# Optimization experiments

Hardware: AMD Instinct MI355X
Metric: run time of the kernel (lower is better)

## Reference

```python
import jax, jax.numpy as jnp
import numpy as np

N_CH = 62
F_DIM = 16
T_DIM = 32
B_DIM = 256
N_NODES = B_DIM * N_CH  # 15872
E_DIM = 200000
SEQ = T_DIM * F_DIM  # 512


def setup_inputs() -> dict:
    key = jax.random.key(0)
    ks = iter(jax.random.split(key, 40))
    s = 0.05
    inp = {}
    inp['x'] = jax.random.normal(next(ks), (N_NODES, F_DIM, T_DIM), dtype=jnp.float32)
    inp['edge_index'] = jax.random.randint(next(ks), (T_DIM, 2, E_DIM), 0, N_NODES, dtype=jnp.int64)
    inp['edge_weight'] = jax.random.uniform(next(ks), (T_DIM, E_DIM), dtype=jnp.float32)
    inp['batch'] = jax.random.randint(next(ks), (T_DIM, N_NODES), 0, B_DIM, dtype=jnp.int64)
    # ChebConv params (K=2): lins have no bias, single bias added at end
    for p in ['c1', 'c2']:
        inp[p + '_w0'] = jax.random.normal(next(ks), (F_DIM, F_DIM), dtype=jnp.float32) * s
        inp[p + '_w1'] = jax.random.normal(next(ks), (F_DIM, F_DIM), dtype=jnp.float32) * s
        inp[p + '_b'] = jnp.zeros((F_DIM,), jnp.float32)
    # LSTM params (torch gate order i,f,g,o); fold b_ih+b_hh into one bias
    for name, i_dim, h_dim in [('l1', N_CH, 64), ('l2', 64, 128), ('l3', 128, 256)]:
        inp[name + '_wih'] = jax.random.normal(next(ks), (4 * h_dim, i_dim), dtype=jnp.float32) * s
        inp[name + '_whh'] = jax.random.normal(next(ks), (4 * h_dim, h_dim), dtype=jnp.float32) * s
        inp[name + '_b'] = jnp.zeros((4 * h_dim,), jnp.float32)
    # MLP head
    for name, i_dim, o_dim in [('fc1', SEQ * 256, 256), ('fc2', 256, 128), ('fc3', 128, 64), ('fc4', 64, 4)]:
        inp[name + '_w'] = jax.random.normal(next(ks), (i_dim, o_dim), dtype=jnp.float32) * s
        inp[name + '_b'] = jnp.zeros((o_dim,), jnp.float32)
    return inp


def _cheb(x, src, dst, w, w0, w1, b):
    # PyG ChebConv K=2, sym norm, lambda_max=2: Tx1 = -D^{-1/2} A D^{-1/2} x
    n = x.shape[0]
    deg = jax.ops.segment_sum(w, src, num_segments=n)
    dinv = jnp.where(deg > 0, jax.lax.rsqrt(deg), 0.0)
    norm = -dinv[src] * w * dinv[dst]
    tx1 = jax.ops.segment_sum(norm[:, None] * x[src], dst, num_segments=n)
    return x @ w0 + tx1 @ w1 + b


def _lstm(x, wih, whh, b):
    # x: [B, S, I] -> [B, S, H], batch_first, zero init state
    bsz, _, _ = x.shape
    h_dim = whh.shape[1]
    xg = x @ wih.T + b  # precompute input gates [B, S, 4H]
    def step(carry, xt):
        h, c = carry
        g = xt + h @ whh.T
        i, f, gg, o = jnp.split(g, 4, axis=-1)
        c = jax.nn.sigmoid(f) * c + jax.nn.sigmoid(i) * jnp.tanh(gg)
        h = jax.nn.sigmoid(o) * jnp.tanh(c)
        return (h, c), h
    h0 = jnp.zeros((bsz, h_dim), x.dtype)
    _, hs = jax.lax.scan(step, (h0, h0), jnp.swapaxes(xg, 0, 1))
    return jnp.swapaxes(hs, 0, 1)


def reference(x, edge_index, edge_weight, batch,
              c1_w0, c1_w1, c1_b, c2_w0, c2_w1, c2_b,
              l1_wih, l1_whh, l1_b, l2_wih, l2_whh, l2_b, l3_wih, l3_whh, l3_b,
              fc1_w, fc1_b, fc2_w, fc2_b, fc3_w, fc3_b, fc4_w, fc4_b):
    def per_t(xt, ei, w):
        h = _cheb(xt, ei[0], ei[1], w, c1_w0, c1_w1, c1_b)
        h = jax.nn.leaky_relu(h, 0.01)
        return _cheb(h, ei[0], ei[1], w, c2_w0, c2_w1, c2_b)
    xt_first = jnp.moveaxis(x, -1, 0)  # [T, N, F]
    h = jax.vmap(per_t)(xt_first, edge_index, edge_weight)  # [T, N, F]
    xc = jnp.moveaxis(h, 0, -1)  # [N, F, T]
    xc = xc.reshape(B_DIM, N_CH, F_DIM, T_DIM)
    xc = jnp.transpose(xc, (0, 3, 2, 1))  # [B, T, F, 62]
    xc = xc.reshape(B_DIM, T_DIM * F_DIM, N_CH)  # [B, S, 62]
    h = _lstm(xc, l1_wih, l1_whh, l1_b)
    h = _lstm(h, l2_wih, l2_whh, l2_b)
    h = _lstm(h, l3_wih, l3_whh, l3_b)
    z = h.reshape(B_DIM, -1)  # [B, S*256]
    z = jax.nn.relu(z @ fc1_w + fc1_b)
    z = jax.nn.relu(z @ fc2_w + fc2_b)
    z = jax.nn.relu(z @ fc3_w + fc3_b)
    return z @ fc4_w + fc4_b
```

## Files before the change

kernel.cpp:

```cpp
#include <hip/hip_runtime.h>
#include <cstdint>
#include <cstddef>


#define T_DIM 32
#define F_DIMC 16
#define NNODE 15872
#define EDGES 200000
#define BATCH 256
#define SEQL 512
#define TN (T_DIM * NNODE)
#define TE (T_DIM * EDGES)
#define ESEG 25000

typedef unsigned short ushortT;
typedef __bf16 bf16_t;
typedef bf16_t bf16x8 __attribute__((ext_vector_type(8)));
typedef float f32x4 __attribute__((ext_vector_type(4)));

__device__ __forceinline__ ushortT f2bf(float f) {
  union { float f; unsigned u; } v; v.f = f;
  unsigned u = v.u;
  u += 0x7fffu + ((u >> 16) & 1u);
  return (ushortT)(u >> 16);
}
__device__ __forceinline__ float fsig(float x) { return 1.0f / (1.0f + __expf(-x)); }
__device__ __forceinline__ float ftanh(float x) {
  float e = __expf(2.0f * x);
  return 1.0f - 2.0f / (e + 1.0f);
}
#define PIN(v) asm volatile("" : "+v"(v))

__device__ __forceinline__ void bar_sync() {
  asm volatile("s_waitcnt lgkmcnt(0)\n\ts_barrier" ::: "memory");
  __builtin_amdgcn_sched_barrier(0);
}

__global__ void k_wprep(const float* __restrict__ w1i, const float* __restrict__ w1h,
                        const float* __restrict__ w2i, const float* __restrict__ w2h,
                        const float* __restrict__ w3i, const float* __restrict__ w3h,
                        ushortT* __restrict__ Wcat) {
  int id = blockIdx.x * 256 + threadIdx.x;
  if (id >= 524288) return;
  float v;
  if (id < 32768) {
    int g = id >> 7, k = id & 127;
    v = (k < 62) ? w1i[g * 62 + k] : ((k >= 64) ? w1h[g * 64 + (k - 64)] : 0.0f);
  } else if (id < 131072) {
    int j = id - 32768; int g = j / 192, k = j % 192;
    v = (k < 64) ? w2i[g * 64 + k] : w2h[g * 128 + (k - 64)];
  } else {
    int j = id - 131072; int g = j / 384, k = j % 384;
    v = (k < 128) ? w3i[g * 128 + k] : w3h[g * 256 + (k - 128)];
  }
  Wcat[id] = f2bf(v);
}

__global__ void k_transpose(const float* __restrict__ x, float* __restrict__ xt) {
  __shared__ float s[528];
  int n = blockIdx.x;
  int tid = threadIdx.x;
  for (int i = tid; i < 512; i += 256) {
    s[(i >> 5) * 33 + (i & 31)] = x[(size_t)n * 512 + i];
  }
  __syncthreads();
  for (int i = tid; i < 512; i += 256) {
    int t = i >> 4, f = i & 15;
    xt[((size_t)t * NNODE + n) * 16 + f] = s[f * 33 + t];
  }
}

__global__ __launch_bounds__(1024, 1) void k_hist8(const int* __restrict__ ei,
                                                   const float* __restrict__ ew,
                                                   float* __restrict__ pdeg,
                                                   int* __restrict__ pcnt,
                                                   int* __restrict__ rank) {
  __shared__ float sdeg[NNODE];
  __shared__ int scnt[NNODE];
  int t = blockIdx.x >> 3;
  int b = blockIdx.x & 7;
  int tid = threadIdx.x;
  for (int i = tid; i < NNODE; i += 1024) { sdeg[i] = 0.0f; scnt[i] = 0; }
  __syncthreads();
  const int* srcp = ei + (size_t)(2 * t) * EDGES;
  const int* dstp = ei + (size_t)(2 * t + 1) * EDGES;
  const float* ewp = ew + (size_t)t * EDGES;
  int* rankp = rank + (size_t)t * EDGES;
  int e0 = b * ESEG, e1 = e0 + ESEG;
  for (int e = e0 + tid; e < e1; e += 1024) {
    int src = srcp[e];
    int dst = dstp[e];
    float w = ewp[e];
    atomicAdd(&sdeg[src], w);
    rankp[e] = atomicAdd(&scnt[dst], 1);
  }
  __syncthreads();
  float* pd = pdeg + (size_t)blockIdx.x * NNODE;
  int* pc = pcnt + (size_t)blockIdx.x * NNODE;
  for (int i = tid; i < NNODE; i += 1024) {
    pd[i] = sdeg[i];
    pc[i] = scnt[i];
  }
}

__global__ void k_merge(const float* __restrict__ pdeg, const int* __restrict__ pcnt,
                        float* __restrict__ deg, int* __restrict__ counts,
                        int* __restrict__ bko) {
  int gid = blockIdx.x * 256 + threadIdx.x;
  if (gid >= TN) return;
  int t = gid / NNODE, n = gid % NNODE;
  int base = t * 8;
  float d = 0.0f;
  int s = 0;
  int pref[8];
#pragma unroll
  for (int b = 0; b < 8; ++b) {
    pref[b] = s;
    d += pdeg[(size_t)(base + b) * NNODE + n];
    s += pcnt[(size_t)(base + b) * NNODE + n];
  }
#pragma unroll
  for (int b = 0; b < 8; ++b) bko[(size_t)gid * 8 + b] = pref[b];
  deg[gid] = d;
  counts[gid] = s;
}

__global__ void k_scanA(const int* __restrict__ counts, int* __restrict__ offs,
                        int* __restrict__ ctot, float* __restrict__ deg) {
  __shared__ int s[256];
  int tid = threadIdx.x;
  int gid = blockIdx.x * 256 + tid;
  float d = deg[gid];
  int v = counts[gid];
  s[tid] = v; __syncthreads();
  for (int off = 1; off < 256; off <<= 1) {
    int x = (tid >= off) ? s[tid - off] : 0;
    __syncthreads();
    s[tid] += x;
    __syncthreads();
  }
  offs[gid] = s[tid] - v;
  if (tid == 255) ctot[blockIdx.x] = s[255];
  deg[gid] = (d > 0.0f) ? rsqrtf(d) : 0.0f;
}

__global__ void k_scanB(const int* __restrict__ ctot, int* __restrict__ cbase) {
  __shared__ int s[256];
  int tid = threadIdx.x;
  int carry = 0;
  for (int c = 0; c < 8; ++c) {
    int i = c * 256 + tid;
    int v = (i < 1984) ? ctot[i] : 0;
    s[tid] = v; __syncthreads();
    for (int off = 1; off < 256; off <<= 1) {
      int x = (tid >= off) ? s[tid - off] : 0;
      __syncthreads();
      s[tid] += x;
      __syncthreads();
    }
    if (i < 1984) cbase[i] = carry + s[tid] - v;
    int tot = s[255];
    __syncthreads();
    carry += tot;
  }
}

__global__ void k_fill2(const int* __restrict__ ei, const float* __restrict__ ew,
                        const float* __restrict__ dinv, const int* __restrict__ offs,
                        const int* __restrict__ cbase, const int* __restrict__ bko,
                        const int* __restrict__ rank,
                        int* __restrict__ csrs, float* __restrict__ csrn) {
  int id = blockIdx.x * 256 + threadIdx.x;
  if (id >= TE) return;
  int t = id / EDGES, e = id % EDGES;
  int src = ei[(size_t)(2 * t) * EDGES + e];
  int dst = ei[(size_t)(2 * t + 1) * EDGES + e];
  int idx = t * NNODE + dst;
  int seg = e / ESEG;
  int pos = offs[idx] + cbase[idx >> 8] + bko[(size_t)idx * 8 + seg] + rank[id];
  csrs[pos] = src;
  csrn[pos] = -dinv[t * NNODE + src] * ew[id] * dinv[idx];
}

__device__ __forceinline__ void fma4(float4& a, float sc, const float4 b) {
  a.x += sc * b.x; a.y += sc * b.y; a.z += sc * b.z; a.w += sc * b.w;
}

__global__ void k_gc(const float* __restrict__ in, const int* __restrict__ offs,
                     const int* __restrict__ cbase,
                     const int* __restrict__ csrs, const float* __restrict__ csrn,
                     const float* __restrict__ w0, const float* __restrict__ w1,
                     const float* __restrict__ bias, float* __restrict__ outF,
                     ushortT* __restrict__ outX, int mode) {
  __shared__ float sw0[256], sw1[256], sb[16];
  int tid = threadIdx.x;
  sw0[tid] = w0[tid];
  sw1[tid] = w1[tid];
  if (tid < 16) sb[tid] = bias[tid];
  __syncthreads();
  int idx = blockIdx.x * 256 + tid;
  if (idx >= TN) return;
  int t = idx / NNODE, n = idx % NNODE;
  const float4* rowp = (const float4*)(in + (size_t)idx * 16);
  float4 x0 = rowp[0], x1 = rowp[1], x2 = rowp[2], x3 = rowp[3];
  float4 a0 = {0, 0, 0, 0}, a1 = {0, 0, 0, 0}, a2 = {0, 0, 0, 0}, a3 = {0, 0, 0, 0};
  int beg = offs[idx] + cbase[idx >> 8];
  int end = (idx == TN - 1) ? TE : offs[idx + 1] + cbase[(idx + 1) >> 8];
  const float* base = in + (size_t)t * NNODE * 16;
  for (int p2 = beg; p2 < end; ++p2) {
    int s = csrs[p2];
    float nr = csrn[p2];
    const float4* rp = (const float4*)(base + (size_t)s * 16);
    fma4(a0, nr, rp[0]); fma4(a1, nr, rp[1]); fma4(a2, nr, rp[2]); fma4(a3, nr, rp[3]);
  }
  float xr[16], ar[16];
  *(float4*)&xr[0] = x0; *(float4*)&xr[4] = x1; *(float4*)&xr[8] = x2; *(float4*)&xr[12] = x3;
  *(float4*)&ar[0] = a0; *(float4*)&ar[4] = a1; *(float4*)&ar[8] = a2; *(float4*)&ar[12] = a3;
  float o[16];
#pragma unroll
  for (int j = 0; j < 16; ++j) o[j] = sb[j];
#pragma unroll
  for (int k = 0; k < 16; ++k) {
    float xv = xr[k], av = ar[k];
#pragma unroll
    for (int j = 0; j < 16; ++j) o[j] += xv * sw0[k * 16 + j] + av * sw1[k * 16 + j];
  }
  if (mode == 0) {
#pragma unroll
    for (int j = 0; j < 16; ++j) o[j] = (o[j] > 0.0f) ? o[j] : 0.01f * o[j];
    float4* op = (float4*)(outF + (size_t)idx * 16);
    op[0] = *(float4*)&o[0]; op[1] = *(float4*)&o[4];
    op[2] = *(float4*)&o[8]; op[3] = *(float4*)&o[12];
  } else {
    int bb = n / 62, ch = n % 62;
#pragma unroll
    for (int j = 0; j < 16; ++j)
      outX[((size_t)(bb * 512 + t * 16 + j)) * 64 + ch] = f2bf(o[j]);
    if (ch < 2) {
#pragma unroll
      for (int j = 0; j < 16; ++j)
        outX[((size_t)(bb * 512 + t * 16 + j)) * 64 + 62 + ch] = 0;
    }
  }
}

__global__ __launch_bounds__(512, 1) void k_lstm(const ushortT* __restrict__ xc,
                                                 const ushortT* __restrict__ Wcat,
                                                 const float* __restrict__ b1g,
                                                 const float* __restrict__ b2g,
                                                 const float* __restrict__ b3g,
                                                 ushortT* __restrict__ zbuf,
                                                 uint32_t* __restrict__ h2x,
                                                 uint32_t* __restrict__ xbuf) {
  __shared__ ushortT X1[2][16 * 72];
  __shared__ ushortT H1[2][16 * 72];
  __shared__ ushortT H2[2][16 * 136];
  __shared__ ushortT HS[2][16 * 136];
  __shared__ ushortT PS[2][16 * 136];
  __shared__ ushortT H2S[2][16 * 136];
  int tid = threadIdx.x;
  int wv = tid >> 6, lane = tid & 63;
  int col = lane & 15, koff = (lane >> 4) * 8, m = lane & 15;
  int bx = blockIdx.x;

  if (bx < 16) {
    int g = bx;
    int bg = g * 16;
    const ushortT* W1 = Wcat;
    const ushortT* W2 = Wcat + 32768;

    bf16x8 w1r[4][4];
    if (wv < 4) {
#pragma unroll
      for (int q = 0; q < 4; ++q)
#pragma unroll
        for (int k = 0; k < 4; ++k) {
          w1r[q][k] = *reinterpret_cast<const bf16x8*>(
              &W1[(size_t)(q * 64 + wv * 16 + col) * 128 + k * 32 + koff]);
          PIN(w1r[q][k]);
        }
    }
    bf16x8 w2r[4][6];
#pragma unroll
    for (int q = 0; q < 4; ++q)
#pragma unroll
      for (int k = 0; k < 6; ++k) {
        w2r[q][k] = *reinterpret_cast<const bf16x8*>(
            &W2[(size_t)(q * 128 + wv * 16 + col) * 192 + k * 32 + koff]);
        PIN(w2r[q][k]);
      }
    float b1v[4] = {0, 0, 0, 0}, b2v[4];
    if (wv < 4) {
#pragma unroll
      for (int q = 0; q < 4; ++q) b1v[q] = b1g[q * 64 + wv * 16 + col];
    }
#pragma unroll
    for (int q = 0; q < 4; ++q) b2v[q] = b2g[q * 128 + wv * 16 + col];

    float c1r[4] = {0, 0, 0, 0};
    float c2r[4] = {0, 0, 0, 0};

    for (int i = tid; i < 2 * 16 * 72; i += 512) { X1[0][i] = 0; H1[0][i] = 0; }
    for (int i = tid; i < 2 * 16 * 136; i += 512) H2[0][i] = 0;
    __syncthreads();
    uint4 xreg = {0, 0, 0, 0};
    {
      int tid2 = tid - 256;
      if (tid2 >= 0 && tid2 < 128) {
        int mm = tid2 >> 3, jj = (tid2 & 7) * 8;
        *(uint4*)&X1[0][mm * 72 + jj] =
            *(const uint4*)&xc[((size_t)(bg + mm) * 512 + 0) * 64 + jj];
        xreg = *(const uint4*)&xc[((size_t)(bg + mm) * 512 + 1) * 64 + jj];
      }
    }
    __syncthreads();

    uint32_t* h2g = h2x + (size_t)g * 512 * 2048;

    for (int t = 0; t < 512; ++t) {
      int pr = t & 1, pw = 1 - pr;
      if (wv < 4) {
        f32x4 acc[4] = {};
#pragma unroll
        for (int kt = 0; kt < 4; ++kt) {
          const ushortT* ap = (kt < 2) ? &X1[pr][m * 72 + kt * 32 + koff]
                                       : &H1[pr][m * 72 + (kt - 2) * 32 + koff];
          bf16x8 a = *reinterpret_cast<const bf16x8*>(ap);
#pragma unroll
          for (int q = 0; q < 4; ++q)
            acc[q] = __builtin_amdgcn_mfma_f32_16x16x32_bf16(a, w1r[q][kt], acc[q], 0, 0, 0);
        }
#pragma unroll
        for (int r = 0; r < 4; ++r) {
          int row = (lane >> 4) * 4 + r;
          int lc = wv * 16 + col;
          float gi = acc[0][r] + b1v[0];
          float gf = acc[1][r] + b1v[1];
          float gg = acc[2][r] + b1v[2];
          float go = acc[3][r] + b1v[3];
          float c = fsig(gf) * c1r[r] + fsig(gi) * ftanh(gg);
          float h = fsig(go) * ftanh(c);
          c1r[r] = c;
          H1[pw][row * 72 + lc] = f2bf(h);
        }
      } else {
        int tid2 = tid - 256;
        if (tid2 < 128) {
          int mm = tid2 >> 3, jj = (tid2 & 7) * 8;
          if (t + 1 < 512)
            *(uint4*)&X1[pw][mm * 72 + jj] = xreg;
          int tf = (t + 2 < 512) ? t + 2 : 511;
          xreg = *(const uint4*)&xc[((size_t)(bg + mm) * 512 + tf) * 64 + jj];
        }
      }
      bar_sync();
      {
        f32x4 acc[4] = {};
#pragma unroll
        for (int kt = 0; kt < 6; ++kt) {
          const ushortT* ap = (kt < 2) ? &H1[pw][m * 72 + kt * 32 + koff]
                                       : &H2[pr][m * 136 + (kt - 2) * 32 + koff];
          bf16x8 a = *reinterpret_cast<const bf16x8*>(ap);
#pragma unroll
          for (int q = 0; q < 4; ++q)
            acc[q] = __builtin_amdgcn_mfma_f32_16x16x32_bf16(a, w2r[q][kt], acc[q], 0, 0, 0);
        }
        uint32_t tag = ((uint32_t)(t + 1)) << 16;
#pragma unroll
        for (int r = 0; r < 4; ++r) {
          int row = (lane >> 4) * 4 + r;
          int lc = wv * 16 + col;
          float gi = acc[0][r] + b2v[0];
          float gf = acc[1][r] + b2v[1];
          float gg = acc[2][r] + b2v[2];
          float go = acc[3][r] + b2v[3];
          float c = fsig(gf) * c2r[r] + fsig(gi) * ftanh(gg);
          float h = fsig(go) * ftanh(c);
          c2r[r] = c;
          ushortT hb = f2bf(h);
          H2[pw][row * 136 + lc] = hb;
          __hip_atomic_store(&h2g[(size_t)t * 2048 + row * 128 + lc], tag | hb,
                             __ATOMIC_RELAXED, __HIP_MEMORY_SCOPE_AGENT);
        }
      }
      bar_sync();
    }
  } else {
    int bxx = bx - 16;
    int s = (bxx >> 3) & 1;
    int g = (bxx & 7) | ((bxx >> 4) << 3);
    int ps = 1 - s;
    int bg = g * 16;
    const ushortT* W3 = Wcat + 131072;

    bf16x8 wH[4][4], wO[4][4], wP[4][4];
#pragma unroll
    for (int q = 0; q < 4; ++q) {
      const ushortT* rw = &W3[(size_t)(q * 256 + s * 128 + wv * 16 + col) * 384];
#pragma unroll
      for (int j = 0; j < 4; ++j) {
        wH[q][j] = *reinterpret_cast<const bf16x8*>(&rw[j * 32 + koff]);
        wO[q][j] = *reinterpret_cast<const bf16x8*>(&rw[(4 + s * 4 + j) * 32 + koff]);
        wP[q][j] = *reinterpret_cast<const bf16x8*>(&rw[(4 + ps * 4 + j) * 32 + koff]);
        PIN(wH[q][j]); PIN(wO[q][j]); PIN(wP[q][j]);
      }
    }
    float b3v[4];
#pragma unroll
    for (int q = 0; q < 4; ++q) b3v[q] = b3g[q * 256 + s * 128 + wv * 16 + col];

    float c3r[4] = {0, 0, 0, 0};

    for (int i = tid; i < 2 * 16 * 136; i += 512) HS[0][i] = 0;
    __syncthreads();

    uint32_t* myslot = xbuf + (((size_t)g * 2 + s) * 2) * 2048;
    const uint32_t* pslot = xbuf + (((size_t)g * 2 + ps) * 2) * 2048;
    const uint32_t* h2g = h2x + (size_t)g * 512 * 2048;

    int prow = tid >> 5, pc0 = (tid & 31) * 4;

    {
      const uint32_t* hp = h2g + prow * 128 + pc0;
      uint32_t u0 = __hip_atomic_load(hp + 0, __ATOMIC_RELAXED, __HIP_MEMORY_SCOPE_AGENT);
      uint32_t u1 = __hip_atomic_load(hp + 1, __ATOMIC_RELAXED, __HIP_MEMORY_SCOPE_AGENT);
      uint32_t u2 = __hip_atomic_load(hp + 2, __ATOMIC_RELAXED, __HIP_MEMORY_SCOPE_AGENT);
      uint32_t u3 = __hip_atomic_load(hp + 3, __ATOMIC_RELAXED, __HIP_MEMORY_SCOPE_AGENT);
      for (;;) {
        bool ok = ((u0 >> 16) == 1u) & ((u1 >> 16) == 1u) &
                  ((u2 >> 16) == 1u) & ((u3 >> 16) == 1u);
        if (ok) break;
        u0 = __hip_atomic_load(hp + 0, __ATOMIC_RELAXED, __HIP_MEMORY_SCOPE_AGENT);
        u1 = __hip_atomic_load(hp + 1, __ATOMIC_RELAXED, __HIP_MEMORY_SCOPE_AGENT);
        u2 = __hip_atomic_load(hp + 2, __ATOMIC_RELAXED, __HIP_MEMORY_SCOPE_AGENT);
        u3 = __hip_atomic_load(hp + 3, __ATOMIC_RELAXED, __HIP_MEMORY_SCOPE_AGENT);
      }
      H2S[0][prow * 136 + pc0 + 0] = (ushortT)(u0 & 0xffffu);
      H2S[0][prow * 136 + pc0 + 1] = (ushortT)(u1 & 0xffffu);
      H2S[0][prow * 136 + pc0 + 2] = (ushortT)(u2 & 0xffffu);
      H2S[0][prow * 136 + pc0 + 3] = (ushortT)(u3 & 0xffffu);
    }
    __syncthreads();

    for (int t = 0; t < 512; ++t) {
      int prt = t & 1, pw = 1 - prt;
      const uint32_t* pb = pslot + (size_t)prt * 2048 + prow * 128 + pc0;
      uint32_t v0 = 0, v1 = 0, v2 = 0, v3 = 0;
      if (t > 0) {
        v0 = __hip_atomic_load(pb + 0, __ATOMIC_RELAXED, __HIP_MEMORY_SCOPE_AGENT);
        v1 = __hip_atomic_load(pb + 1, __ATOMIC_RELAXED, __HIP_MEMORY_SCOPE_AGENT);
        v2 = __hip_atomic_load(pb + 2, __ATOMIC_RELAXED, __HIP_MEMORY_SCOPE_AGENT);
        v3 = __hip_atomic_load(pb + 3, __ATOMIC_RELAXED, __HIP_MEMORY_SCOPE_AGENT);
      }
      const uint32_t* hp = h2g + (size_t)(t + 1) * 2048 + prow * 128 + pc0;
      uint32_t u0 = 0, u1 = 0, u2 = 0, u3 = 0;
      if (t < 511) {
        u0 = __hip_atomic_load(hp + 0, __ATOMIC_RELAXED, __HIP_MEMORY_SCOPE_AGENT);
        u1 = __hip_atomic_load(hp + 1, __ATOMIC_RELAXED, __HIP_MEMORY_SCOPE_AGENT);
        u2 = __hip_atomic_load(hp + 2, __ATOMIC_RELAXED, __HIP_MEMORY_SCOPE_AGENT);
        u3 = __hip_atomic_load(hp + 3, __ATOMIC_RELAXED, __HIP_MEMORY_SCOPE_AGENT);
      }
      __builtin_amdgcn_sched_barrier(0);
      f32x4 acc[4] = {};
#pragma unroll
      for (int kt = 0; kt < 4; ++kt) {
        bf16x8 a = *reinterpret_cast<const bf16x8*>(&H2S[prt][m * 136 + kt * 32 + koff]);
#pragma unroll
        for (int q = 0; q < 4; ++q)
          acc[q] = __builtin_amdgcn_mfma_f32_16x16x32_bf16(a, wH[q][kt], acc[q], 0, 0, 0);
      }
      if (t > 0) {
#pragma unroll
        for (int j = 0; j < 4; ++j) {
          bf16x8 a = *reinterpret_cast<const bf16x8*>(&HS[prt][m * 136 + j * 32 + koff]);
#pragma unroll
          for (int q = 0; q < 4; ++q)
            acc[q] = __builtin_amdgcn_mfma_f32_16x16x32_bf16(a, wO[q][j], acc[q], 0, 0, 0);
        }
        {
          uint32_t want = (uint32_t)t;
          while (((v0 >> 16) != want) | ((v1 >> 16) != want) |
                 ((v2 >> 16) != want) | ((v3 >> 16) != want)) {
            v0 = __hip_atomic_load(pb + 0, __ATOMIC_RELAXED, __HIP_MEMORY_SCOPE_AGENT);
            v1 = __hip_atomic_load(pb + 1, __ATOMIC_RELAXED, __HIP_MEMORY_SCOPE_AGENT);
            v2 = __hip_atomic_load(pb + 2, __ATOMIC_RELAXED, __HIP_MEMORY_SCOPE_AGENT);
            v3 = __hip_atomic_load(pb + 3, __ATOMIC_RELAXED, __HIP_MEMORY_SCOPE_AGENT);
          }
          PS[prt][prow * 136 + pc0 + 0] = (ushortT)(v0 & 0xffffu);
          PS[prt][prow * 136 + pc0 + 1] = (ushortT)(v1 & 0xffffu);
          PS[prt][prow * 136 + pc0 + 2] = (ushortT)(v2 & 0xffffu);
          PS[prt][prow * 136 + pc0 + 3] = (ushortT)(v3 & 0xffffu);
        }
        bar_sync();
#pragma unroll
        for (int j = 0; j < 4; ++j) {
          bf16x8 a = *reinterpret_cast<const bf16x8*>(&PS[prt][m * 136 + j * 32 + koff]);
#pragma unroll
          for (int q = 0; q < 4; ++q)
            acc[q] = __builtin_amdgcn_mfma_f32_16x16x32_bf16(a, wP[q][j], acc[q], 0, 0, 0);
        }
      }
      if (t < 511) {
        uint32_t want = (uint32_t)(t + 2);
        while (((u0 >> 16) != want) | ((u1 >> 16) != want) |
               ((u2 >> 16) != want) | ((u3 >> 16) != want)) {
          u0 = __hip_atomic_load(hp + 0, __ATOMIC_RELAXED, __HIP_MEMORY_SCOPE_AGENT);
          u1 = __hip_atomic_load(hp + 1, __ATOMIC_RELAXED, __HIP_MEMORY_SCOPE_AGENT);
          u2 = __hip_atomic_load(hp + 2, __ATOMIC_RELAXED, __HIP_MEMORY_SCOPE_AGENT);
          u3 = __hip_atomic_load(hp + 3, __ATOMIC_RELAXED, __HIP_MEMORY_SCOPE_AGENT);
        }
        H2S[pw][prow * 136 + pc0 + 0] = (ushortT)(u0 & 0xffffu);
        H2S[pw][prow * 136 + pc0 + 1] = (ushortT)(u1 & 0xffffu);
        H2S[pw][prow * 136 + pc0 + 2] = (ushortT)(u2 & 0xffffu);
        H2S[pw][prow * 136 + pc0 + 3] = (ushortT)(u3 & 0xffffu);
      }
      uint32_t* mw = myslot + (size_t)((t + 1) & 1) * 2048;
      ushortT hbs[4];
#pragma unroll
      for (int r = 0; r < 4; ++r) {
        int row = (lane >> 4) * 4 + r;
        int lc = wv * 16 + col;
        float gi = acc[0][r] + b3v[0];
        float gf = acc[1][r] + b3v[1];
        float gg = acc[2][r] + b3v[2];
        float go = acc[3][r] + b3v[3];
        float c = fsig(gf) * c3r[r] + fsig(gi) * ftanh(gg);
        float h = fsig(go) * ftanh(c);
        c3r[r] = c;
        hbs[r] = f2bf(h);
        __hip_atomic_store(mw + row * 128 + lc, ((uint32_t)(t + 1) << 16) | hbs[r],
                           __ATOMIC_RELAXED, __HIP_MEMORY_SCOPE_AGENT);
      }
      asm volatile("s_waitcnt vmcnt(0)" ::: "memory");
      __builtin_amdgcn_sched_barrier(0);
#pragma unroll
      for (int r = 0; r < 4; ++r) {
        int row = (lane >> 4) * 4 + r;
        int lc = wv * 16 + col;
        HS[pw][row * 136 + lc] = hbs[r];
        zbuf[((size_t)(bg + row) * 512 + t) * 256 + s * 128 + lc] = hbs[r];
      }
      bar_sync();
    }
  }
}

__global__ __launch_bounds__(256) void k_fc1(const ushortT* __restrict__ zbuf,
                                             const float* __restrict__ w,
                                             float* __restrict__ part) {
  __shared__ ushortT As[256 * 40];
  __shared__ ushortT Bs[64 * 40];
  int tid = threadIdx.x;
  int kb = blockIdx.x;
  int nb = blockIdx.y;
  int wv = tid >> 6, lane = tid & 63;
  int col = lane & 15, koff = (lane >> 4) * 8;
  int k0base = kb * 2048;
  f32x4 acc[4][4] = {};
  for (int kt = 0; kt < 64; ++kt) {
    int k0 = k0base + kt * 32;
    {
      const uint4* src = (const uint4*)(zbuf + (size_t)tid * 131072 + k0);
      uint4* dst = (uint4*)(As + tid * 40);
      dst[0] = src[0]; dst[1] = src[1]; dst[2] = src[2]; dst[3] = src[3];
    }
    {
      int kk = tid >> 3, j0 = (tid & 7) * 8;
      const float* srcw = w + (size_t)(k0 + kk) * 256 + nb * 64 + j0;
#pragma unroll
      for (int jj = 0; jj < 8; ++jj) Bs[(j0 + jj) * 40 + kk] = f2bf(srcw[jj]);
    }
    __syncthreads();
    bf16x8 bfr[4];
#pragma unroll
    for (int nt = 0; nt < 4; ++nt)
      bfr[nt] = *reinterpret_cast<const bf16x8*>(&Bs[(nt * 16 + col) * 40 + koff]);
#pragma unroll
    for (int mt = 0; mt < 4; ++mt) {
      bf16x8 afr = *reinterpret_cast<const bf16x8*>(&As[(wv * 64 + mt * 16 + col) * 40 + koff]);
#pragma unroll
      for (int nt = 0; nt < 4; ++nt)
        acc[mt][nt] = __builtin_amdgcn_mfma_f32_16x16x32_bf16(afr, bfr[nt], acc[mt][nt], 0, 0, 0);
    }
    __syncthreads();
  }
#pragma unroll
  for (int mt = 0; mt < 4; ++mt)
#pragma unroll
    for (int nt = 0; nt < 4; ++nt)
#pragma unroll
      for (int r = 0; r < 4; ++r) {
        int m = wv * 64 + mt * 16 + (lane >> 4) * 4 + r;
        int n = nb * 64 + nt * 16 + col;
        part[(size_t)kb * 65536 + m * 256 + n] = acc[mt][nt][r];
      }
}

__global__ void k_fc1red(const float* __restrict__ part, const float* __restrict__ b,
                         float* __restrict__ out) {
  int id4 = blockIdx.x * 256 + threadIdx.x;
  if (id4 >= 16384) return;
  float4 s = {0.0f, 0.0f, 0.0f, 0.0f};
  for (int kb = 0; kb < 64; ++kb) {
    float4 v = *(const float4*)&part[(size_t)kb * 65536 + id4 * 4];
    s.x += v.x; s.y += v.y; s.z += v.z; s.w += v.w;
  }
  int n0 = (id4 * 4) & 255;
  s.x = fmaxf(s.x + b[n0 + 0], 0.0f);
  s.y = fmaxf(s.y + b[n0 + 1], 0.0f);
  s.z = fmaxf(s.z + b[n0 + 2], 0.0f);
  s.w = fmaxf(s.w + b[n0 + 3], 0.0f);
  *(float4*)&out[id4 * 4] = s;
}

__global__ void k_fcv(const float* __restrict__ in, const float* __restrict__ w,
                      const float* __restrict__ b, float* __restrict__ out,
                      int K, int Nn, int doRelu) {
  int id = blockIdx.x * 256 + threadIdx.x;
  int m = id / Nn, n = id % Nn;
  float s = b[n];
  for (int k = 0; k < K; ++k) s += in[m * K + k] * w[k * Nn + n];
  if (doRelu) s = fmaxf(s, 0.0f);
  out[id] = s;
}

extern "C" void kernel_launch(void* const* d_in, const int* in_sizes, int n_in,
                              void* d_out, int out_size, void* d_ws, size_t ws_size,
                              hipStream_t stream) {
  (void)in_sizes; (void)n_in; (void)out_size; (void)ws_size;
  const float* x    = (const float*)d_in[0];
  const int* ei     = (const int*)d_in[1];
  const float* ew   = (const float*)d_in[2];
  const float* c1w0 = (const float*)d_in[4];
  const float* c1w1 = (const float*)d_in[5];
  const float* c1b  = (const float*)d_in[6];
  const float* c2w0 = (const float*)d_in[7];
  const float* c2w1 = (const float*)d_in[8];
  const float* c2b  = (const float*)d_in[9];
  const float* l1wi = (const float*)d_in[10];
  const float* l1wh = (const float*)d_in[11];
  const float* l1b  = (const float*)d_in[12];
  const float* l2wi = (const float*)d_in[13];
  const float* l2wh = (const float*)d_in[14];
  const float* l2b  = (const float*)d_in[15];
  const float* l3wi = (const float*)d_in[16];
  const float* l3wh = (const float*)d_in[17];
  const float* l3b  = (const float*)d_in[18];
  const float* fc1w = (const float*)d_in[19];
  const float* fc1b = (const float*)d_in[20];
  const float* fc2w = (const float*)d_in[21];
  const float* fc2b = (const float*)d_in[22];
  const float* fc3w = (const float*)d_in[23];
  const float* fc3b = (const float*)d_in[24];
  const float* fc4w = (const float*)d_in[25];
  const float* fc4b = (const float*)d_in[26];
  float* out = (float*)d_out;

  char* p = (char*)d_ws;
  auto alloc = [&](size_t bytes) { void* r = (void*)p; p += (bytes + 255) & ~(size_t)255; return r; };
  float* xt      = (float*)alloc(32505856);
  float* h1buf   = (float*)alloc(32505856);
  float* dinv    = (float*)alloc(2031616);
  int* counts    = (int*)alloc(2031616);
  int* offs      = (int*)alloc(2031616);
  int* fillc     = (int*)alloc(2031616);
  int* ctot      = (int*)alloc(8192);
  int* cbase     = (int*)alloc(8192);
  int* csrs      = (int*)alloc(25600000);
  float* csrn    = (float*)alloc(25600000);
  ushortT* xc    = (ushortT*)alloc(16777216);
  ushortT* Wcat  = (ushortT*)alloc(1048576);
  ushortT* zbuf  = (ushortT*)alloc(67108864);
  float* part    = (float*)alloc(16777216);
  float* fo1     = (float*)alloc(262144);
  float* fo2     = (float*)alloc(131072);
  float* fo3     = (float*)alloc(65536);
  uint32_t* xbuf = (uint32_t*)alloc(524288);
  (void)fillc;
  int* rank = (int*)h1buf;
  uint32_t* h2x = (uint32_t*)xt;
  float* pdeg = (float*)zbuf;
  int* pcnt = (int*)((char*)zbuf + 16777216);
  int* bko = (int*)((char*)zbuf + 35127296);


  k_wprep<<<2048, 256, 0, stream>>>(l1wi, l1wh, l2wi, l2wh, l3wi, l3wh, Wcat);
  k_transpose<<<15872, 256, 0, stream>>>(x, xt);
  k_hist8<<<256, 1024, 0, stream>>>(ei, ew, pdeg, pcnt, rank);
  k_merge<<<1984, 256, 0, stream>>>(pdeg, pcnt, dinv, counts, bko);
  k_scanA<<<1984, 256, 0, stream>>>(counts, offs, ctot, dinv);
  k_scanB<<<1, 256, 0, stream>>>(ctot, cbase);
  k_fill2<<<25000, 256, 0, stream>>>(ei, ew, dinv, offs, cbase, bko, rank, csrs, csrn);
  k_gc<<<1984, 256, 0, stream>>>(xt, offs, cbase, csrs, csrn, c1w0, c1w1, c1b, h1buf, nullptr, 0);
  k_gc<<<1984, 256, 0, stream>>>(h1buf, offs, cbase, csrs, csrn, c2w0, c2w1, c2b, nullptr, xc, 1);
  hipMemsetAsync(h2x, 0, 67108864, stream);
  k_lstm<<<48, 512, 0, stream>>>(xc, Wcat, l1b, l2b, l3b, zbuf, h2x, xbuf);
  k_fc1<<<dim3(64, 4), 256, 0, stream>>>(zbuf, fc1w, part);
  k_fc1red<<<64, 256, 0, stream>>>(part, fc1b, fo1);
  k_fcv<<<128, 256, 0, stream>>>(fo1, fc2w, fc2b, fo2, 256, 128, 1);
  k_fcv<<<64, 256, 0, stream>>>(fo2, fc3w, fc3b, fo3, 128, 64, 1);
  k_fcv<<<4, 256, 0, stream>>>(fo3, fc4w, fc4b, out, 64, 4, 0);
}
```

Baseline: 3.008 ms.

## Overlap second ChebConv with LSTM via tagged producer blocks in one mega kernel

Merges the second graph convolution into the LSTM launch. 208 extra blocks compute the conv per timestep and write tagged 32-bit values into xc. The LSTM blocks spin-wait on those tags before consuming each input row, so the LSTM can start as soon as early timesteps are ready. This hides the second conv behind the serial recurrence. The cost is twice the xc footprint, an extra memset, and a dependence on all 256 blocks being co-resident to avoid deadlock.

Result: faster. 2.934 ms (-2.5%).

```diff
diff --git a/kernel.cpp b/kernel.cpp
--- a/kernel.cpp
+++ b/kernel.cpp
@@ -12,6 +12,7 @@
 #define TN (T_DIM * NNODE)
 #define TE (T_DIM * EDGES)
 #define ESEG 25000
+#define NWORK 208
 
 typedef unsigned short ushortT;
 typedef __bf16 bf16_t;
@@ -34,6 +35,13 @@
 __device__ __forceinline__ void bar_sync() {
   asm volatile("s_waitcnt lgkmcnt(0)\n\ts_barrier" ::: "memory");
   __builtin_amdgcn_sched_barrier(0);
+}
+
+__device__ __forceinline__ uint32_t aload(const uint32_t* p) {
+  return __hip_atomic_load(p, __ATOMIC_RELAXED, __HIP_MEMORY_SCOPE_AGENT);
+}
+__device__ __forceinline__ void astore(uint32_t* p, uint32_t v) {
+  __hip_atomic_store(p, v, __ATOMIC_RELAXED, __HIP_MEMORY_SCOPE_AGENT);
 }
 
 __global__ void k_wprep(const float* __restrict__ w1i, const float* __restrict__ w1h,
@@ -186,12 +194,11 @@
   a.x += sc * b.x; a.y += sc * b.y; a.z += sc * b.z; a.w += sc * b.w;
 }
 
-__global__ void k_gc(const float* __restrict__ in, const int* __restrict__ offs,
-                     const int* __restrict__ cbase,
-                     const int* __restrict__ csrs, const float* __restrict__ csrn,
-                     const float* __restrict__ w0, const float* __restrict__ w1,
-                     const float* __restrict__ bias, float* __restrict__ outF,
-                     ushortT* __restrict__ outX, int mode) {
+__global__ void k_gc1(const float* __restrict__ in, const int* __restrict__ offs,
+                      const int* __restrict__ cbase,
+                      const int* __restrict__ csrs, const float* __restrict__ csrn,
+                      const float* __restrict__ w0, const float* __restrict__ w1,
+                      const float* __restrict__ bias, float* __restrict__ outF) {
   __shared__ float sw0[256], sw1[256], sb[16];
   int tid = threadIdx.x;
   sw0[tid] = w0[tid];
@@ -200,7 +207,7 @@
   __syncthreads();
   int idx = blockIdx.x * 256 + tid;
   if (idx >= TN) return;
-  int t = idx / NNODE, n = idx % NNODE;
+  int t = idx / NNODE;
   const float4* rowp = (const float4*)(in + (size_t)idx * 16);
   float4 x0 = rowp[0], x1 = rowp[1], x2 = rowp[2], x3 = rowp[3];
   float4 a0 = {0, 0, 0, 0}, a1 = {0, 0, 0, 0}, a2 = {0, 0, 0, 0}, a3 = {0, 0, 0, 0};
@@ -225,43 +232,86 @@
 #pragma unroll
     for (int j = 0; j < 16; ++j) o[j] += xv * sw0[k * 16 + j] + av * sw1[k * 16 + j];
   }
-  if (mode == 0) {
-#pragma unroll
-    for (int j = 0; j < 16; ++j) o[j] = (o[j] > 0.0f) ? o[j] : 0.01f * o[j];
-    float4* op = (float4*)(outF + (size_t)idx * 16);
-    op[0] = *(float4*)&o[0]; op[1] = *(float4*)&o[4];
-    op[2] = *(float4*)&o[8]; op[3] = *(float4*)&o[12];
-  } else {
-    int bb = n / 62, ch = n % 62;
-#pragma unroll
-    for (int j = 0; j < 16; ++j)
-      outX[((size_t)(bb * 512 + t * 16 + j)) * 64 + ch] = f2bf(o[j]);
-    if (ch < 2) {
-#pragma unroll
-      for (int j = 0; j < 16; ++j)
-        outX[((size_t)(bb * 512 + t * 16 + j)) * 64 + 62 + ch] = 0;
-    }
-  }
-}
-
-__global__ __launch_bounds__(512, 1) void k_lstm(const ushortT* __restrict__ xc,
-                                                 const ushortT* __restrict__ Wcat,
-                                                 const float* __restrict__ b1g,
-                                                 const float* __restrict__ b2g,
-                                                 const float* __restrict__ b3g,
-                                                 ushortT* __restrict__ zbuf,
-                                                 uint32_t* __restrict__ h2x,
-                                                 uint32_t* __restrict__ xbuf) {
+#pragma unroll
+  for (int j = 0; j < 16; ++j) o[j] = (o[j] > 0.0f) ? o[j] : 0.01f * o[j];
+  float4* op = (float4*)(outF + (size_t)idx * 16);
+  op[0] = *(float4*)&o[0]; op[1] = *(float4*)&o[4];
+  op[2] = *(float4*)&o[8]; op[3] = *(float4*)&o[12];
+}
+
+__global__ __launch_bounds__(512, 1) void k_mega(
+    const uint32_t* __restrict__ xc32_c, uint32_t* __restrict__ xc32,
+    const ushortT* __restrict__ Wcat,
+    const float* __restrict__ b1g, const float* __restrict__ b2g,
+    const float* __restrict__ b3g,
+    ushortT* __restrict__ zbuf, uint32_t* __restrict__ h2x,
+    uint32_t* __restrict__ xbuf,
+    const float* __restrict__ h1buf, const int* __restrict__ offs,
+    const int* __restrict__ cbase, const int* __restrict__ csrs,
+    const float* __restrict__ csrn,
+    const float* __restrict__ c2w0, const float* __restrict__ c2w1,
+    const float* __restrict__ c2b) {
   __shared__ ushortT X1[2][16 * 72];
   __shared__ ushortT H1[2][16 * 72];
   __shared__ ushortT H2[2][16 * 136];
   __shared__ ushortT HS[2][16 * 136];
   __shared__ ushortT PS[2][16 * 136];
   __shared__ ushortT H2S[2][16 * 136];
+  __shared__ float swa[256], swb[256], sbb[16];
   int tid = threadIdx.x;
   int wv = tid >> 6, lane = tid & 63;
   int col = lane & 15, koff = (lane >> 4) * 8, m = lane & 15;
   int bx = blockIdx.x;
+
+  if (bx >= 48) {
+    if (tid < 256) { swa[tid] = c2w0[tid]; swb[tid] = c2w1[tid]; }
+    if (tid < 16) sbb[tid] = c2b[tid];
+    __syncthreads();
+    int wtid = (bx - 48) * 512 + tid;
+    for (int t = 0; t < 32; ++t) {
+      uint32_t tag = ((uint32_t)(t + 1)) << 16;
+      const float* h1t = h1buf + (size_t)t * NNODE * 16;
+      const int* csrsp = csrs;
+      const float* csrnp = csrn;
+      for (int n = wtid; n < NNODE; n += NWORK * 512) {
+        int idx = t * NNODE + n;
+        int beg = offs[idx] + cbase[idx >> 8];
+        int end = (idx == TN - 1) ? TE : offs[idx + 1] + cbase[(idx + 1) >> 8];
+        const float4* rowp = (const float4*)(h1t + (size_t)n * 16);
+        float4 x0 = rowp[0], x1 = rowp[1], x2 = rowp[2], x3 = rowp[3];
+        float4 a0 = {0, 0, 0, 0}, a1 = {0, 0, 0, 0}, a2 = {0, 0, 0, 0}, a3 = {0, 0, 0, 0};
+        const float* basei = h1buf + (size_t)t * NNODE * 16;
+        for (int p2 = beg; p2 < end; ++p2) {
+          int s = csrsp[p2];
+          float nr = csrnp[p2];
+          const float4* rp = (const float4*)(basei + (size_t)s * 16);
+          fma4(a0, nr, rp[0]); fma4(a1, nr, rp[1]); fma4(a2, nr, rp[2]); fma4(a3, nr, rp[3]);
+        }
+        float xr[16], ar[16];
+        *(float4*)&xr[0] = x0; *(float4*)&xr[4] = x1; *(float4*)&xr[8] = x2; *(float4*)&xr[12] = x3;
+        *(float4*)&ar[0] = a0; *(float4*)&ar[4] = a1; *(float4*)&ar[8] = a2; *(float4*)&ar[12] = a3;
+        float o[16];
+#pragma unroll
+        for (int j = 0; j < 16; ++j) o[j] = sbb[j];
+#pragma unroll
+        for (int k = 0; k < 16; ++k) {
+          float xv = xr[k], av = ar[k];
+#pragma unroll
+          for (int j = 0; j < 16; ++j) o[j] += xv * swa[k * 16 + j] + av * swb[k * 16 + j];
+        }
+        int bb = n / 62, ch = n % 62;
+#pragma unroll
+        for (int j = 0; j < 16; ++j)
+          astore(&xc32[((size_t)(bb * 512 + t * 16 + j)) * 64 + ch], tag | f2bf(o[j]));
+        if (ch < 2) {
+#pragma unroll
+          for (int j = 0; j < 16; ++j)
+            astore(&xc32[((size_t)(bb * 512 + t * 16 + j)) * 64 + 62 + ch], tag);
+        }
+      }
+    }
+    return;
+  }
 
   if (bx < 16) {
     int g = bx;
@@ -308,9 +358,37 @@
       int tid2 = tid - 256;
       if (tid2 >= 0 && tid2 < 128) {
         int mm = tid2 >> 3, jj = (tid2 & 7) * 8;
-        *(uint4*)&X1[0][mm * 72 + jj] =
-            *(const uint4*)&xc[((size_t)(bg + mm) * 512 + 0) * 64 + jj];
-        xreg = *(const uint4*)&xc[((size_t)(bg + mm) * 512 + 1) * 64 + jj];
+        const uint32_t* p0 = &xc32_c[((size_t)(bg + mm) * 512 + 0) * 64 + jj];
+        uint32_t w[8];
+#pragma unroll
+        for (int i = 0; i < 8; ++i) w[i] = aload(p0 + i);
+        for (;;) {
+          bool ok = true;
+#pragma unroll
+          for (int i = 0; i < 8; ++i)
+            if ((w[i] >> 16) != 1u) { ok = false; w[i] = aload(p0 + i); }
+          if (ok) break;
+        }
+        uint4 v;
+        v.x = (w[0] & 0xffffu) | (w[1] << 16);
+        v.y = (w[2] & 0xffffu) | (w[3] << 16);
+        v.z = (w[4] & 0xffffu) | (w[5] << 16);
+        v.w = (w[6] & 0xffffu) | (w[7] << 16);
+        *(uint4*)&X1[0][mm * 72 + jj] = v;
+        const uint32_t* p1 = &xc32_c[((size_t)(bg + mm) * 512 + 1) * 64 + jj];
+#pragma unroll
+        for (int i = 0; i < 8; ++i) w[i] = aload(p1 + i);
+        for (;;) {
+          bool ok = true;
+#pragma unroll
+          for (int i = 0; i < 8; ++i)
+            if ((w[i] >> 16) != 1u) { ok = false; w[i] = aload(p1 + i); }
+          if (ok) break;
+        }
+        xreg.x = (w[0] & 0xffffu) | (w[1] << 16);
+        xreg.y = (w[2] & 0xffffu) | (w[3] << 16);
+        xreg.z = (w[4] & 0xffffu) | (w[5] << 16);
+        xreg.w = (w[6] & 0xffffu) | (w[7] << 16);
       }
     }
     __syncthreads();
@@ -350,7 +428,22 @@
           if (t + 1 < 512)
             *(uint4*)&X1[pw][mm * 72 + jj] = xreg;
           int tf = (t + 2 < 512) ? t + 2 : 511;
-          xreg = *(const uint4*)&xc[((size_t)(bg + mm) * 512 + tf) * 64 + jj];
+          const uint32_t* pp = &xc32_c[((size_t)(bg + mm) * 512 + tf) * 64 + jj];
+          uint32_t want = (uint32_t)((tf >> 4) + 1);
+          uint32_t w[8];
+#pragma unroll
+          for (int i = 0; i < 8; ++i) w[i] = aload(pp + i);
+          for (;;) {
+            bool ok = true;
+#pragma unroll
+            for (int i = 0; i < 8; ++i)
+              if ((w[i] >> 16) != want) { ok = false; w[i] = aload(pp + i); }
+            if (ok) break;
+          }
+          xreg.x = (w[0] & 0xffffu) | (w[1] << 16);
+          xreg.y = (w[2] & 0xffffu) | (w[3] << 16);
+          xreg.z = (w[4] & 0xffffu) | (w[5] << 16);
+          xreg.w = (w[6] & 0xffffu) | (w[7] << 16);
         }
       }
       bar_sync();
@@ -379,8 +472,7 @@
           c2r[r] = c;
           ushortT hb = f2bf(h);
           H2[pw][row * 136 + lc] = hb;
-          __hip_atomic_store(&h2g[(size_t)t * 2048 + row * 128 + lc], tag | hb,
-                             __ATOMIC_RELAXED, __HIP_MEMORY_SCOPE_AGENT);
+          astore(&h2g[(size_t)t * 2048 + row * 128 + lc], tag | hb);
         }
       }
       bar_sync();
@@ -422,18 +514,12 @@
 
     {
       const uint32_t* hp = h2g + prow * 128 + pc0;
-      uint32_t u0 = __hip_atomic_load(hp + 0, __ATOMIC_RELAXED, __HIP_MEMORY_SCOPE_AGENT);
-      uint32_t u1 = __hip_atomic_load(hp + 1, __ATOMIC_RELAXED, __HIP_MEMORY_SCOPE_AGENT);
-      uint32_t u2 = __hip_atomic_load(hp + 2, __ATOMIC_RELAXED, __HIP_MEMORY_SCOPE_AGENT);
-      uint32_t u3 = __hip_atomic_load(hp + 3, __ATOMIC_RELAXED, __HIP_MEMORY_SCOPE_AGENT);
+      uint32_t u0 = aload(hp + 0), u1 = aload(hp + 1), u2 = aload(hp + 2), u3 = aload(hp + 3);
       for (;;) {
         bool ok = ((u0 >> 16) == 1u) & ((u1 >> 16) == 1u) &
                   ((u2 >> 16) == 1u) & ((u3 >> 16) == 1u);
         if (ok) break;
-        u0 = __hip_atomic_load(hp + 0, __ATOMIC_RELAXED, __HIP_MEMORY_SCOPE_AGENT);
-        u1 = __hip_atomic_load(hp + 1, __ATOMIC_RELAXED, __HIP_MEMORY_SCOPE_AGENT);
-        u2 = __hip_atomic_load(hp + 2, __ATOMIC_RELAXED, __HIP_MEMORY_SCOPE_AGENT);
-        u3 = __hip_atomic_load(hp + 3, __ATOMIC_RELAXED, __HIP_MEMORY_SCOPE_AGENT);
+        u0 = aload(hp + 0); u1 = aload(hp + 1); u2 = aload(hp + 2); u3 = aload(hp + 3);
       }
       H2S[0][prow * 136 + pc0 + 0] = (ushortT)(u0 & 0xffffu);
       H2S[0][prow * 136 + pc0 + 1] = (ushortT)(u1 & 0xffffu);
@@ -447,18 +533,12 @@
       const uint32_t* pb = pslot + (size_t)prt * 2048 + prow * 128 + pc0;
       uint32_t v0 = 0, v1 = 0, v2 = 0, v3 = 0;
       if (t > 0) {
-        v0 = __hip_atomic_load(pb + 0, __ATOMIC_RELAXED, __HIP_MEMORY_SCOPE_AGENT);
-        v1 = __hip_atomic_load(pb + 1, __ATOMIC_RELAXED, __HIP_MEMORY_SCOPE_AGENT);
-        v2 = __hip_atomic_load(pb + 2, __ATOMIC_RELAXED, __HIP_MEMORY_SCOPE_AGENT);
-        v3 = __hip_atomic_load(pb + 3, __ATOMIC_RELAXED, __HIP_MEMORY_SCOPE_AGENT);
+        v0 = aload(pb + 0); v1 = aload(pb + 1); v2 = aload(pb + 2); v3 = aload(pb + 3);
       }
       const uint32_t* hp = h2g + (size_t)(t + 1) * 2048 + prow * 128 + pc0;
       uint32_t u0 = 0, u1 = 0, u2 = 0, u3 = 0;
       if (t < 511) {
-        u0 = __hip_atomic_load(hp + 0, __ATOMIC_RELAXED, __HIP_MEMORY_SCOPE_AGENT);
-        u1 = __hip_atomic_load(hp + 1, __ATOMIC_RELAXED, __HIP_MEMORY_SCOPE_AGENT);
-        u2 = __hip_atomic_load(hp + 2, __ATOMIC_RELAXED, __HIP_MEMORY_SCOPE_AGENT);
-        u3 = __hip_atomic_load(hp + 3, __ATOMIC_RELAXED, __HIP_MEMORY_SCOPE_AGENT);
+        u0 = aload(hp + 0); u1 = aload(hp + 1); u2 = aload(hp + 2); u3 = aload(hp + 3);
       }
       __builtin_amdgcn_sched_barrier(0);
       f32x4 acc[4] = {};
@@ -481,10 +561,7 @@
           uint32_t want = (uint32_t)t;
           while (((v0 >> 16) != want) | ((v1 >> 16) != want) |
                  ((v2 >> 16) != want) | ((v3 >> 16) != want)) {
-            v0 = __hip_atomic_load(pb + 0, __ATOMIC_RELAXED, __HIP_MEMORY_SCOPE_AGENT);
-            v1 = __hip_atomic_load(pb + 1, __ATOMIC_RELAXED, __HIP_MEMORY_SCOPE_AGENT);
-            v2 = __hip_atomic_load(pb + 2, __ATOMIC_RELAXED, __HIP_MEMORY_SCOPE_AGENT);
-            v3 = __hip_atomic_load(pb + 3, __ATOMIC_RELAXED, __HIP_MEMORY_SCOPE_AGENT);
+            v0 = aload(pb + 0); v1 = aload(pb + 1); v2 = aload(pb + 2); v3 = aload(pb + 3);
           }
           PS[prt][prow * 136 + pc0 + 0] = (ushortT)(v0 & 0xffffu);
           PS[prt][prow * 136 + pc0 + 1] = (ushortT)(v1 & 0xffffu);
@@ -504,10 +581,7 @@
         uint32_t want = (uint32_t)(t + 2);
         while (((u0 >> 16) != want) | ((u1 >> 16) != want) |
                ((u2 >> 16) != want) | ((u3 >> 16) != want)) {
-          u0 = __hip_atomic_load(hp + 0, __ATOMIC_RELAXED, __HIP_MEMORY_SCOPE_AGENT);
-          u1 = __hip_atomic_load(hp + 1, __ATOMIC_RELAXED, __HIP_MEMORY_SCOPE_AGENT);
-          u2 = __hip_atomic_load(hp + 2, __ATOMIC_RELAXED, __HIP_MEMORY_SCOPE_AGENT);
-          u3 = __hip_atomic_load(hp + 3, __ATOMIC_RELAXED, __HIP_MEMORY_SCOPE_AGENT);
+          u0 = aload(hp + 0); u1 = aload(hp + 1); u2 = aload(hp + 2); u3 = aload(hp + 3);
         }
         H2S[pw][prow * 136 + pc0 + 0] = (ushortT)(u0 & 0xffffu);
         H2S[pw][prow * 136 + pc0 + 1] = (ushortT)(u1 & 0xffffu);
@@ -528,8 +602,7 @@
         float h = fsig(go) * ftanh(c);
         c3r[r] = c;
         hbs[r] = f2bf(h);
-        __hip_atomic_store(mw + row * 128 + lc, ((uint32_t)(t + 1) << 16) | hbs[r],
-                           __ATOMIC_RELAXED, __HIP_MEMORY_SCOPE_AGENT);
+        astore(mw + row * 128 + lc, ((uint32_t)(t + 1) << 16) | hbs[r]);
       }
       asm volatile("s_waitcnt vmcnt(0)" ::: "memory");
       __builtin_amdgcn_sched_barrier(0);
@@ -663,12 +736,11 @@
   float* dinv    = (float*)alloc(2031616);
   int* counts    = (int*)alloc(2031616);
   int* offs      = (int*)alloc(2031616);
-  int* fillc     = (int*)alloc(2031616);
   int* ctot      = (int*)alloc(8192);
   int* cbase     = (int*)alloc(8192);
   int* csrs      = (int*)alloc(25600000);
   float* csrn    = (float*)alloc(25600000);
-  ushortT* xc    = (ushortT*)alloc(16777216);
+  uint32_t* xc32 = (uint32_t*)alloc(33554432);
   ushortT* Wcat  = (ushortT*)alloc(1048576);
   ushortT* zbuf  = (ushortT*)alloc(67108864);
   float* part    = (float*)alloc(16777216);
@@ -676,13 +748,14 @@
   float* fo2     = (float*)alloc(131072);
   float* fo3     = (float*)alloc(65536);
   uint32_t* xbuf = (uint32_t*)alloc(524288);
-  (void)fillc;
+  uint32_t* h2x = (uint32_t*)alloc(67108864);
   int* rank = (int*)h1buf;
-  uint32_t* h2x = (uint32_t*)xt;
   float* pdeg = (float*)zbuf;
   int* pcnt = (int*)((char*)zbuf + 16777216);
   int* bko = (int*)((char*)zbuf + 35127296);
 
+  hipMemsetAsync(h2x, 0, 67108864, stream);
+  hipMemsetAsync(xc32, 0, 33554432, stream);
 
   k_wprep<<<2048, 256, 0, stream>>>(l1wi, l1wh, l2wi, l2wh, l3wi, l3wh, Wcat);
   k_transpose<<<15872, 256, 0, stream>>>(x, xt);
@@ -691,10 +764,10 @@
   k_scanA<<<1984, 256, 0, stream>>>(counts, offs, ctot, dinv);
   k_scanB<<<1, 256, 0, stream>>>(ctot, cbase);
   k_fill2<<<25000, 256, 0, stream>>>(ei, ew, dinv, offs, cbase, bko, rank, csrs, csrn);
-  k_gc<<<1984, 256, 0, stream>>>(xt, offs, cbase, csrs, csrn, c1w0, c1w1, c1b, h1buf, nullptr, 0);
-  k_gc<<<1984, 256, 0, stream>>>(h1buf, offs, cbase, csrs, csrn, c2w0, c2w1, c2b, nullptr, xc, 1);
-  hipMemsetAsync(h2x, 0, 67108864, stream);
-  k_lstm<<<48, 512, 0, stream>>>(xc, Wcat, l1b, l2b, l3b, zbuf, h2x, xbuf);
+  k_gc1<<<1984, 256, 0, stream>>>(xt, offs, cbase, csrs, csrn, c1w0, c1w1, c1b, h1buf);
+  k_mega<<<256, 512, 0, stream>>>(xc32, xc32, Wcat, l1b, l2b, l3b, zbuf, h2x,
+                                  xbuf, h1buf, offs, cbase, csrs, csrn,
+                                  c2w0, c2w1, c2b);
   k_fc1<<<dim3(64, 4), 256, 0, stream>>>(zbuf, fc1w, part);
   k_fc1red<<<64, 256, 0, stream>>>(part, fc1b, fo1);
   k_fcv<<<128, 256, 0, stream>>>(fo1, fc2w, fc2b, fo2, 256, 128, 1);
```
